# Kernel optimization log

Measured on AMD Instinct MI355X. Metric: run time of the kernel, lower is better.

## Reference

```python
import jax, jax.numpy as jnp
import numpy as np

D_MODEL = 1024
NUM_HEADS = 16
D_K = D_MODEL // NUM_HEADS


def setup_inputs() -> dict:
    key = jax.random.key(0)
    ks = jax.random.split(key, 5)
    s = 1.0 / np.sqrt(D_MODEL)
    return {
        "x": jax.random.normal(ks[0], (2, 2048, D_MODEL), dtype=jnp.float32),
        "Wq": jax.random.normal(ks[1], (D_MODEL, D_MODEL), dtype=jnp.float32) * s,
        "bq": jnp.zeros((D_MODEL,), dtype=jnp.float32),
        "Wk": jax.random.normal(ks[2], (D_MODEL, D_MODEL), dtype=jnp.float32) * s,
        "bk": jnp.zeros((D_MODEL,), dtype=jnp.float32),
        "Wv": jax.random.normal(ks[3], (D_MODEL, D_MODEL), dtype=jnp.float32) * s,
        "bv": jnp.zeros((D_MODEL,), dtype=jnp.float32),
        "Wo": jax.random.normal(ks[4], (D_MODEL, D_MODEL), dtype=jnp.float32) * s,
        "bo": jnp.zeros((D_MODEL,), dtype=jnp.float32),
    }


def reference(x, Wq, bq, Wk, bk, Wv, bv, Wo, bo):
    B, S, D = x.shape
    H, dk = NUM_HEADS, D_K
    Q = x @ Wq + bq  # [B, S, D]
    K = x @ Wk + bk
    V = x @ Wv + bv
    # Faithful to the torch code: plain .view(B, H, S, dk) (NO transpose),
    # i.e. heads are carved out of the flattened (S*D) dim, not the feature dim.
    Q = Q.reshape(B, H, S, dk)
    K = K.reshape(B, H, S, dk)
    V = V.reshape(B, H, S, dk)
    scores = jnp.einsum("bhqd,bhkd->bhqk", Q, K) / jnp.sqrt(jnp.float32(dk))
    attn = jax.nn.softmax(scores, axis=-1)  # [B, H, S, S]
    ctx = jnp.einsum("bhqk,bhkd->bhqd", attn, V)  # [B, H, S, dk]
    out = ctx.reshape(B, S, D) @ Wo + bo
    return out  # dropout is identity in eval mode
```

## Files before the change

### kernel.cpp

```cpp
#include <hip/hip_runtime.h>
#include <hip/hip_bf16.h>
#include <math.h>

#define D_MODEL 1024
#define SEQ     2048
#define BATCH   2
#define NHEAD   16
#define DKH     64
#define BH      (BATCH * NHEAD)

typedef unsigned short u16;
typedef unsigned int   u32;
typedef __bf16 bf16x8 __attribute__((ext_vector_type(8)));
typedef float  f32x4  __attribute__((ext_vector_type(4)));

#define MFMA16(a, b, c) __builtin_amdgcn_mfma_f32_16x16x32_bf16((a), (b), (c), 0, 0, 0)
#define AS1 __attribute__((address_space(1)))
#define AS3 __attribute__((address_space(3)))

#define QSCALE 0.18033688f

__device__ __forceinline__ u16 f2bf(float x) {
    u32 u = __float_as_uint(x);
    u += 0x7fffu + ((u >> 16) & 1u);
    return (u16)(u >> 16);
}
__device__ __forceinline__ float bf2f(u16 b) {
    return __uint_as_float(((u32)b) << 16);
}
__device__ __forceinline__ void gl16(const u16* g, void* lds) {
    __builtin_amdgcn_global_load_lds((const AS1 u32*)g, (AS3 u32*)lds, 16, 0, 0);
}

__global__ __launch_bounds__(256) void conv_all(
    const float* __restrict__ x, u16* __restrict__ Xh, int n4,
    const float* __restrict__ W0, const float* __restrict__ W1,
    const float* __restrict__ W2, const float* __restrict__ W3,
    u16* __restrict__ H0, u16* __restrict__ L0, u16* __restrict__ H1, u16* __restrict__ L1,
    u16* __restrict__ H2, u16* __restrict__ L2, u16* __restrict__ H3, u16* __restrict__ L3)
{
    const int t = threadIdx.x;
    if ((int)blockIdx.x < 4096) {
        int i = blockIdx.x * 256 + t;
        if (i >= n4) return;
        float4 v = reinterpret_cast<const float4*>(x)[i];
        uint2 H;
        H.x = f2bf(v.x) | ((u32)f2bf(v.y) << 16);
        H.y = f2bf(v.z) | ((u32)f2bf(v.w) << 16);
        reinterpret_cast<uint2*>(Xh)[i] = H;
        return;
    }
    int id = blockIdx.x - 4096;
    int bx = id & 15, by = (id >> 4) & 15, bz = id >> 8;
    const float* W; u16 *Ht, *Lt;
    if (bz == 0)      { W = W0; Ht = H0; Lt = L0; }
    else if (bz == 1) { W = W1; Ht = H1; Lt = L1; }
    else if (bz == 2) { W = W2; Ht = H2; Lt = L2; }
    else              { W = W3; Ht = H3; Lt = L3; }

    __shared__ float T[64][65];
    const int n0 = bx * 64, k0 = by * 64;
    #pragma unroll
    for (int i = 0; i < 4; ++i) {
        int f = t + i * 256;
        int kr = f >> 4, ns = (f & 15) * 4;
        float4 v = *reinterpret_cast<const float4*>(&W[(size_t)(k0 + kr) * D_MODEL + n0 + ns]);
        T[kr][ns + 0] = v.x; T[kr][ns + 1] = v.y; T[kr][ns + 2] = v.z; T[kr][ns + 3] = v.w;
    }
    __syncthreads();
    #pragma unroll
    for (int i = 0; i < 4; ++i) {
        int f = t + i * 256;
        int nr = f >> 4, ks = (f & 15) * 4;
        u16 hh[4], ll[4];
        #pragma unroll
        for (int j = 0; j < 4; ++j) {
            float xv = T[ks + j][nr];
            u16 hb = f2bf(xv);
            hh[j] = hb;
            ll[j] = f2bf(xv - bf2f(hb));
        }
        uint2 H, L;
        H.x = hh[0] | ((u32)hh[1] << 16); H.y = hh[2] | ((u32)hh[3] << 16);
        L.x = ll[0] | ((u32)ll[1] << 16); L.y = ll[2] | ((u32)ll[3] << 16);
        size_t o = (size_t)(n0 + nr) * D_MODEL + k0 + ks;
        *reinterpret_cast<uint2*>(&Ht[o]) = H;
        *reinterpret_cast<uint2*>(&Lt[o]) = L;
    }
}

__global__ __launch_bounds__(512, 2) void gemm_qkv(
    const u16* __restrict__ AhG,
    const u16* __restrict__ Bqh, const u16* __restrict__ Bql,
    const u16* __restrict__ Bkh, const u16* __restrict__ Bkl,
    const u16* __restrict__ Bvh, const u16* __restrict__ Bvl,
    const float* __restrict__ bq, const float* __restrict__ bk, const float* __restrict__ bv,
    u16* __restrict__ Qb, u16* __restrict__ Kb, u16* __restrict__ Vb)
{
    constexpr int K = D_MODEL, N = D_MODEL;
    __shared__ u16 LB[2][28672];

    const int tid  = threadIdx.x;
    const int wv   = tid >> 6;
    const int lane = tid & 63;
    const int quad = lane >> 4;
    const int l16  = lane & 15;
    const int wm   = wv & 1, wn = wv >> 1;
    const int brow = blockIdx.y * 128, bcol = blockIdx.x * 128;

    const u16* sp[7];
    int sldb[7];
    #pragma unroll
    for (int j = 0; j < 7; ++j) {
        int c = (j < 3) ? (wv * 3 + j)
              : (j < 5) ? (24 + wv * 2 + (j - 3))
                        : (40 + wv * 2 + (j - 5));
        int a = c >> 3, cc = c & 7;
        int row = cc * 16 + (lane >> 2);
        int gseg = (lane & 3) ^ ((lane >> 3) & 3);
        const u16* p;
        if (a == 0)      p = AhG;
        else if (a == 1) p = Bqh;
        else if (a == 2) p = Bql;
        else if (a == 3) p = Bkh;
        else if (a == 4) p = Bkl;
        else if (a == 5) p = Bvh;
        else             p = Bvl;
        int rbase = (a == 0) ? brow : bcol;
        sp[j]   = p + (size_t)(rbase + row) * K + gseg * 8;
        sldb[j] = a * 8192 + cc * 1024;
    }

    int aro[4], bro[2];
    #pragma unroll
    for (int i = 0; i < 4; ++i) {
        int mr = wm * 64 + i * 16 + l16;
        aro[i] = mr * 64 + ((quad ^ ((mr >> 1) & 3)) * 16);
    }
    #pragma unroll
    for (int i = 0; i < 2; ++i) {
        int nr = wn * 32 + i * 16 + l16;
        bro[i] = nr * 64 + ((quad ^ ((nr >> 1) & 3)) * 16);
    }

    f32x4 acc[3][4][2] = {};

    auto rdB = [&](int cur, int m, bf16x8 (&bh)[2], bf16x8 (&bl)[2]) {
        const int bbh = (1 + 2 * m) * 8192, bbl = (2 + 2 * m) * 8192;
        #pragma unroll
        for (int i = 0; i < 2; ++i) {
            bh[i] = *reinterpret_cast<const bf16x8*>((const char*)LB[cur] + bbh + bro[i]);
            bl[i] = *reinterpret_cast<const bf16x8*>((const char*)LB[cur] + bbl + bro[i]);
        }
    };
    auto mm = [&](int m, bf16x8 (&ah)[4], bf16x8 (&bh)[2], bf16x8 (&bl)[2]) {
        __builtin_amdgcn_s_setprio(1);
        #pragma unroll
        for (int mi = 0; mi < 4; ++mi)
            #pragma unroll
            for (int ni = 0; ni < 2; ++ni) {
                f32x4 c = acc[m][mi][ni];
                c = MFMA16(ah[mi], bh[ni], c);
                c = MFMA16(ah[mi], bl[ni], c);
                acc[m][mi][ni] = c;
            }
        __builtin_amdgcn_s_setprio(0);
    };

    #pragma unroll
    for (int j = 0; j < 7; ++j)
        gl16(sp[j], (char*)LB[0] + sldb[j]);

    for (int it = 0; it < K / 32 - 1; ++it) {
        const int cur = it & 1, nx = cur ^ 1;
        const int k1 = (it + 1) * 32;
        bf16x8 ah[4], bh[2], bl[2];

        asm volatile("s_waitcnt vmcnt(4)" ::: "memory");
        __builtin_amdgcn_s_barrier();
        #pragma unroll
        for (int i = 0; i < 4; ++i)
            ah[i] = *reinterpret_cast<const bf16x8*>((const char*)LB[cur] + aro[i]);
        rdB(cur, 0, bh, bl);
        gl16(sp[0] + k1, (char*)LB[nx] + sldb[0]);
        gl16(sp[1] + k1, (char*)LB[nx] + sldb[1]);
        gl16(sp[2] + k1, (char*)LB[nx] + sldb[2]);
        mm(0, ah, bh, bl);

        asm volatile("s_waitcnt vmcnt(5)" ::: "memory");
        __builtin_amdgcn_s_barrier();
        rdB(cur, 1, bh, bl);
        gl16(sp[3] + k1, (char*)LB[nx] + sldb[3]);
        gl16(sp[4] + k1, (char*)LB[nx] + sldb[4]);
        mm(1, ah, bh, bl);

        asm volatile("s_waitcnt vmcnt(5)" ::: "memory");
        __builtin_amdgcn_s_barrier();
        rdB(cur, 2, bh, bl);
        gl16(sp[5] + k1, (char*)LB[nx] + sldb[5]);
        gl16(sp[6] + k1, (char*)LB[nx] + sldb[6]);
        mm(2, ah, bh, bl);
    }

    {
        const int cur = (K / 32 - 1) & 1;
        bf16x8 ah[4], bh[2], bl[2];

        asm volatile("s_waitcnt vmcnt(4)" ::: "memory");
        __builtin_amdgcn_s_barrier();
        #pragma unroll
        for (int i = 0; i < 4; ++i)
            ah[i] = *reinterpret_cast<const bf16x8*>((const char*)LB[cur] + aro[i]);
        rdB(cur, 0, bh, bl);
        mm(0, ah, bh, bl);

        asm volatile("s_waitcnt vmcnt(2)" ::: "memory");
        __builtin_amdgcn_s_barrier();
        rdB(cur, 1, bh, bl);
        mm(1, ah, bh, bl);

        asm volatile("s_waitcnt vmcnt(0)" ::: "memory");
        __builtin_amdgcn_s_barrier();
        rdB(cur, 2, bh, bl);
        mm(2, ah, bh, bl);
    }

    #pragma unroll
    for (int m = 0; m < 3; ++m) {
        const float* bias = (m == 0) ? bq : (m == 1) ? bk : bv;
        u16* out = (m == 0) ? Qb : (m == 1) ? Kb : Vb;
        const float sc = (m == 0) ? QSCALE : 1.0f;
        #pragma unroll
        for (int mi = 0; mi < 4; ++mi) {
            #pragma unroll
            for (int ni = 0; ni < 2; ++ni) {
                int col = bcol + wn * 32 + ni * 16 + l16;
                float bvv = bias[col];
                #pragma unroll
                for (int r = 0; r < 4; ++r) {
                    int row = brow + wm * 64 + mi * 16 + quad * 4 + r;
                    out[(size_t)row * N + col] = f2bf((acc[m][mi][ni][r] + bvv) * sc);
                }
            }
        }
    }
}

__global__ __launch_bounds__(512, 2) void gemm_oproj(
    const u16* __restrict__ AhG, const u16* __restrict__ Bh, const u16* __restrict__ Bl,
    const float* __restrict__ bias, float* __restrict__ Cf)
{
    constexpr int K = D_MODEL, N = D_MODEL;
    __shared__ u16 LB[2][12288];

    const int tid  = threadIdx.x;
    const int wv   = tid >> 6;
    const int lane = tid & 63;
    const int quad = lane >> 4;
    const int l16  = lane & 15;
    const int wm   = wv & 1, wn = wv >> 1;
    const int brow = blockIdx.y * 128, bcol = blockIdx.x * 128;

    const u16* sp[3];
    int sldb[3];
    #pragma unroll
    for (int j = 0; j < 3; ++j) {
        int c = wv * 3 + j, a = c >> 3, cc = c & 7;
        int row = cc * 16 + (lane >> 2);
        int gseg = (lane & 3) ^ ((lane >> 3) & 3);
        const u16* p = (a == 0) ? AhG : (a == 1) ? Bh : Bl;
        int rbase = (a == 0) ? brow : bcol;
        sp[j]   = p + (size_t)(rbase + row) * K + gseg * 8;
        sldb[j] = a * 8192 + cc * 1024;
    }

    int aro[4], bro[2];
    #pragma unroll
    for (int i = 0; i < 4; ++i) {
        int mr = wm * 64 + i * 16 + l16;
        aro[i] = mr * 64 + ((quad ^ ((mr >> 1) & 3)) * 16);
    }
    #pragma unroll
    for (int i = 0; i < 2; ++i) {
        int nr = wn * 32 + i * 16 + l16;
        bro[i] = nr * 64 + ((quad ^ ((nr >> 1) & 3)) * 16);
    }

    f32x4 acc[4][2] = {};

    #pragma unroll
    for (int j = 0; j < 3; ++j)
        gl16(sp[j], (char*)LB[0] + sldb[j]);

    for (int it = 0; it < K / 32; ++it) {
        const int cur = it & 1;
        __syncthreads();
        if (it + 1 < K / 32) {
            const int nxt = cur ^ 1;
            const int k1 = (it + 1) * 32;
            #pragma unroll
            for (int j = 0; j < 3; ++j)
                gl16(sp[j] + k1, (char*)LB[nxt] + sldb[j]);
        }

        bf16x8 ah[4], bh[2], bl[2];
        #pragma unroll
        for (int i = 0; i < 4; ++i)
            ah[i] = *reinterpret_cast<const bf16x8*>((const char*)LB[cur] + aro[i]);
        #pragma unroll
        for (int i = 0; i < 2; ++i) {
            bh[i] = *reinterpret_cast<const bf16x8*>((const char*)LB[cur] + 8192 + bro[i]);
            bl[i] = *reinterpret_cast<const bf16x8*>((const char*)LB[cur] + 16384 + bro[i]);
        }
        #pragma unroll
        for (int mi = 0; mi < 4; ++mi)
            #pragma unroll
            for (int ni = 0; ni < 2; ++ni) {
                f32x4 c = acc[mi][ni];
                c = MFMA16(ah[mi], bh[ni], c);
                c = MFMA16(ah[mi], bl[ni], c);
                acc[mi][ni] = c;
            }
    }

    #pragma unroll
    for (int mi = 0; mi < 4; ++mi) {
        #pragma unroll
        for (int ni = 0; ni < 2; ++ni) {
            int col = bcol + wn * 32 + ni * 16 + l16;
            float bvv = bias[col];
            #pragma unroll
            for (int r = 0; r < 4; ++r) {
                int row = brow + wm * 64 + mi * 16 + quad * 4 + r;
                Cf[(size_t)row * N + col] = acc[mi][ni][r] + bvv;
            }
        }
    }
}

__global__ __launch_bounds__(256) void v_transpose(
    const u16* __restrict__ V, u16* __restrict__ Vt)
{
    __shared__ u16 T[64][72];
    const int bh = blockIdx.y, st = blockIdx.x;
    const u16* src = V + ((size_t)bh * SEQ + (size_t)st * 64) * 64;
    const int t = threadIdx.x;
    #pragma unroll
    for (int i = 0; i < 2; ++i) {
        int c  = t + i * 256;
        int s  = c >> 3;
        int d0 = (c & 7) * 8;
        uint4 v = reinterpret_cast<const uint4*>(src)[c];
        u16 e[8];
        e[0] = (u16)(v.x & 0xffff); e[1] = (u16)(v.x >> 16);
        e[2] = (u16)(v.y & 0xffff); e[3] = (u16)(v.y >> 16);
        e[4] = (u16)(v.z & 0xffff); e[5] = (u16)(v.z >> 16);
        e[6] = (u16)(v.w & 0xffff); e[7] = (u16)(v.w >> 16);
        #pragma unroll
        for (int j = 0; j < 8; ++j) T[d0 + j][s] = e[j];
    }
    __syncthreads();
    const int d = t >> 2, seg = t & 3;
    u16* dst = Vt + (size_t)bh * 64 * SEQ + (size_t)d * SEQ + st * 64 + seg * 16;
    uint4 a = *reinterpret_cast<const uint4*>(&T[d][seg * 16]);
    uint4 b = *reinterpret_cast<const uint4*>(&T[d][seg * 16 + 8]);
    reinterpret_cast<uint4*>(dst)[0] = a;
    reinterpret_cast<uint4*>(dst)[1] = b;
}

__global__ __launch_bounds__(256, 2) void attn_mfma(
    const u16* __restrict__ Qb_g, const u16* __restrict__ Kb_g,
    const u16* __restrict__ Vt_g, u16* __restrict__ Ch_g)
{
    __shared__ u16 KVS[3][8192];
    __shared__ u16 Pb [128 * 72];

    const int tid  = threadIdx.x;
    const int wv   = tid >> 6;
    const int lane = tid & 63;
    const int quad = lane >> 4;
    const int l16  = lane & 15;
    const int id   = blockIdx.x;
    const int bh   = id & 31;
    const int qt   = id >> 5;

    const size_t qbase = ((size_t)bh * SEQ + (size_t)qt * 128) * 64;
    const size_t kbh   = (size_t)bh * SEQ * 64;
    const size_t vtbh  = (size_t)bh * 64 * SEQ;

    bf16x8 qf[2][2];
    #pragma unroll
    for (int sub = 0; sub < 2; ++sub)
        #pragma unroll
        for (int ks = 0; ks < 2; ++ks) {
            size_t o = qbase + (size_t)(wv * 32 + sub * 16 + l16) * 64 + ks * 32 + quad * 8;
            qf[sub][ks] = *reinterpret_cast<const bf16x8*>(Qb_g + o);
        }

    const u16* sp[4];
    size_t sstep[4];
    int sldb[4];
    #pragma unroll
    for (int j = 0; j < 4; ++j) {
        int c   = wv * 4 + j;
        int arr = c >> 3, cc = c & 7;
        int row = cc * 8 + (lane >> 3);
        int sg  = (lane & 7) ^ (row & 7);
        if (arr == 0) { sp[j] = Kb_g + kbh + (size_t)row * 64 + sg * 8;   sstep[j] = 4096; }
        else          { sp[j] = Vt_g + vtbh + (size_t)row * SEQ + sg * 8; sstep[j] = 64; }
        sldb[j] = arr * 8192 + cc * 1024;
    }

    int fro[4][2];
    #pragma unroll
    for (int t = 0; t < 4; ++t)
        #pragma unroll
        for (int ks = 0; ks < 2; ++ks)
            fro[t][ks] = (t * 16 + l16) * 128 + (((ks * 4 + quad) ^ (l16 & 7)) * 16);

    bf16x8 onesv;
    #pragma unroll
    for (int i = 0; i < 8; ++i) onesv[i] = (__bf16)1.0f;

    f32x4 oacc[2][4] = {};
    f32x4 lsum[2] = {};

    auto S_step = [&](int bufidx, f32x4 (&sacc)[2][4]) {
        const char* kb = (const char*)KVS[bufidx];
        #pragma unroll
        for (int t4 = 0; t4 < 4; ++t4) {
            bf16x8 kh0 = *reinterpret_cast<const bf16x8*>(kb + fro[t4][0]);
            bf16x8 kh1 = *reinterpret_cast<const bf16x8*>(kb + fro[t4][1]);
            #pragma unroll
            for (int sub = 0; sub < 2; ++sub) {
                f32x4 a = sacc[sub][t4];
                a = MFMA16(qf[sub][0], kh0, a);
                a = MFMA16(qf[sub][1], kh1, a);
                sacc[sub][t4] = a;
            }
        }
    };

    auto PV_step = [&](int bufidx) {
        const char* vb = (const char*)KVS[bufidx] + 8192;
        bf16x8 bvf[4][2];
        #pragma unroll
        for (int dt = 0; dt < 4; ++dt) {
            bvf[dt][0] = *reinterpret_cast<const bf16x8*>(vb + fro[dt][0]);
            bvf[dt][1] = *reinterpret_cast<const bf16x8*>(vb + fro[dt][1]);
        }
        #pragma unroll
        for (int sub = 0; sub < 2; ++sub) {
            bf16x8 ap[2];
            #pragma unroll
            for (int ks = 0; ks < 2; ++ks)
                ap[ks] = *reinterpret_cast<const bf16x8*>(
                    &Pb[(wv * 32 + sub * 16 + l16) * 72 + ks * 32 + quad * 8]);
            #pragma unroll
            for (int dt = 0; dt < 4; ++dt) {
                oacc[sub][dt] = MFMA16(ap[0], bvf[dt][0], oacc[sub][dt]);
                oacc[sub][dt] = MFMA16(ap[1], bvf[dt][1], oacc[sub][dt]);
            }
            lsum[sub] = MFMA16(ap[0], onesv, lsum[sub]);
            lsum[sub] = MFMA16(ap[1], onesv, lsum[sub]);
        }
    };

    auto EXP2_step = [&](f32x4 (&sacc)[2][4]) {
        #pragma unroll
        for (int sub = 0; sub < 2; ++sub) {
            int rowb = wv * 32 + sub * 16 + quad * 4;
            #pragma unroll
            for (int r = 0; r < 4; ++r) {
                u32 u0 = __float_as_uint(__builtin_amdgcn_exp2f(sacc[sub][0][r]));
                u32 u1 = __float_as_uint(__builtin_amdgcn_exp2f(sacc[sub][1][r]));
                u32 u2 = __float_as_uint(__builtin_amdgcn_exp2f(sacc[sub][2][r]));
                u32 u3 = __float_as_uint(__builtin_amdgcn_exp2f(sacc[sub][3][r]));
                int ro = (rowb + r) * 72 + l16;
                Pb[ro +  0] = (u16)(u0 >> 16);
                Pb[ro + 16] = (u16)(u1 >> 16);
                Pb[ro + 32] = (u16)(u2 >> 16);
                Pb[ro + 48] = (u16)(u3 >> 16);
            }
        }
    };

    #pragma unroll
    for (int j = 0; j < 4; ++j)
        gl16(sp[j], (char*)KVS[0] + sldb[j]);

    {
        __syncthreads();
        #pragma unroll
        for (int j = 0; j < 4; ++j)
            gl16(sp[j] + sstep[j], (char*)KVS[1] + sldb[j]);
        f32x4 sacc[2][4] = {};
        __builtin_amdgcn_s_setprio(1);
        S_step(0, sacc);
        __builtin_amdgcn_s_setprio(0);
        EXP2_step(sacc);
    }

    int cur = 1, prv = 0, nxt = 2;
    for (int kt = 1; kt < SEQ / 64; ++kt) {
        __syncthreads();
        if (kt + 1 < SEQ / 64) {
            #pragma unroll
            for (int j = 0; j < 4; ++j)
                gl16(sp[j] + (size_t)(kt + 1) * sstep[j], (char*)KVS[nxt] + sldb[j]);
        }

        f32x4 sacc[2][4] = {};
        __builtin_amdgcn_s_setprio(1);
        S_step(cur, sacc);
        PV_step(prv);
        __builtin_amdgcn_s_setprio(0);
        EXP2_step(sacc);

        prv = cur; cur = nxt; nxt = (nxt == 2) ? 0 : nxt + 1;
    }

    __builtin_amdgcn_s_setprio(1);
    PV_step(prv);
    __builtin_amdgcn_s_setprio(0);

    u16* Oh = Ch_g + qbase;
    #pragma unroll
    for (int sub = 0; sub < 2; ++sub) {
        float inv[4];
        #pragma unroll
        for (int r = 0; r < 4; ++r) inv[r] = 1.0f / lsum[sub][r];
        #pragma unroll
        for (int dt = 0; dt < 4; ++dt)
            #pragma unroll
            for (int r = 0; r < 4; ++r) {
                int row = wv * 32 + sub * 16 + quad * 4 + r;
                Oh[(size_t)row * 64 + dt * 16 + l16] = f2bf(oacc[sub][dt][r] * inv[r]);
            }
    }
}

extern "C" void kernel_launch(void* const* d_in, const int* in_sizes, int n_in,
                              void* d_out, int out_size, void* d_ws, size_t ws_size,
                              hipStream_t stream)
{
    const float* x  = (const float*)d_in[0];
    const float* Wq = (const float*)d_in[1];
    const float* bq = (const float*)d_in[2];
    const float* Wk = (const float*)d_in[3];
    const float* bk = (const float*)d_in[4];
    const float* Wv = (const float*)d_in[5];
    const float* bv = (const float*)d_in[6];
    const float* Wo = (const float*)d_in[7];
    const float* bo = (const float*)d_in[8];
    float* out = (float*)d_out;

    const int M = BATCH * SEQ;
    const int N = D_MODEL;
    const size_t NE = (size_t)M * N;
    const size_t NW = (size_t)N * N;

    u16* w16 = (u16*)d_ws;
    u16* Xh   = w16;
    u16* Qb   = Xh   + NE;
    u16* Kb   = Qb   + NE;
    u16* Vb   = Kb   + NE;
    u16* Vtb  = Vb   + NE;
    u16* Ctxh = Vtb  + NE;
    u16* WTqh = Ctxh + NE;
    u16* WTql = WTqh + NW;
    u16* WTkh = WTql + NW;
    u16* WTkl = WTkh + NW;
    u16* WTvh = WTkl + NW;
    u16* WTvl = WTvh + NW;
    u16* WToh = WTvl + NW;
    u16* WTol = WToh + NW;

    conv_all<<<dim3(4096 + 1024), dim3(256), 0, stream>>>(
        x, Xh, (int)(NE / 4),
        Wq, Wk, Wv, Wo, WTqh, WTql, WTkh, WTkl, WTvh, WTvl, WToh, WTol);

    gemm_qkv<<<dim3(N / 128, M / 128), dim3(512), 0, stream>>>(
        Xh, WTqh, WTql, WTkh, WTkl, WTvh, WTvl, bq, bk, bv, Qb, Kb, Vb);

    v_transpose<<<dim3(SEQ / 64, BH), dim3(256), 0, stream>>>(Vb, Vtb);

    attn_mfma<<<dim3((SEQ / 128) * BH), dim3(256), 0, stream>>>(Qb, Kb, Vtb, Ctxh);

    gemm_oproj<<<dim3(N / 128, M / 128), dim3(512), 0, stream>>>(
        Ctxh, WToh, WTol, bo, out);
}
```

Measured before the change: 212.8 us.

## Split attention work across eight waves and pack P and V-transpose stores

The attention kernel now runs 512 threads per block, so each wave handles 16 query rows instead of 32. This halves per-wave accumulator registers and raises the number of waves available to hide latency. The cost is that each K/V fragment read from LDS now feeds half as many MFMAs. The softmax P tile is written as packed 64-bit words using a permuted key order, and the V-transpose kernel writes V in the same permuted order so P·V stays consistent. This replaces scattered 16-bit LDS stores with wider ones.

```diff
diff --git a/kernel.cpp b/kernel.cpp
--- a/kernel.cpp
+++ b/kernel.cpp
@@ -361,14 +361,24 @@
     }
     __syncthreads();
     const int d = t >> 2, seg = t & 3;
-    u16* dst = Vt + (size_t)bh * 64 * SEQ + (size_t)d * SEQ + st * 64 + seg * 16;
-    uint4 a = *reinterpret_cast<const uint4*>(&T[d][seg * 16]);
-    uint4 b = *reinterpret_cast<const uint4*>(&T[d][seg * 16 + 8]);
-    reinterpret_cast<uint4*>(dst)[0] = a;
-    reinterpret_cast<uint4*>(dst)[1] = b;
-}
-
-__global__ __launch_bounds__(256, 2) void attn_mfma(
+    u16* dst = Vt + (size_t)bh * 64 * SEQ + (size_t)d * SEQ + st * 64;
+    #pragma unroll
+    for (int gg = 0; gg < 2; ++gg) {
+        int g = seg * 2 + gg;
+        u32 r0 = *reinterpret_cast<const u32*>(&T[d][2 * g]);
+        u32 r1 = *reinterpret_cast<const u32*>(&T[d][2 * g + 16]);
+        u32 r2 = *reinterpret_cast<const u32*>(&T[d][2 * g + 32]);
+        u32 r3 = *reinterpret_cast<const u32*>(&T[d][2 * g + 48]);
+        uint4 w;
+        w.x = (r0 & 0xffffu) | (r1 << 16);
+        w.y = (r2 & 0xffffu) | (r3 << 16);
+        w.z = (r0 >> 16) | (r1 & 0xffff0000u);
+        w.w = (r2 >> 16) | (r3 & 0xffff0000u);
+        *reinterpret_cast<uint4*>(&dst[8 * g]) = w;
+    }
+}
+
+__global__ __launch_bounds__(512, 4) void attn_mfma(
     const u16* __restrict__ Qb_g, const u16* __restrict__ Kb_g,
     const u16* __restrict__ Vt_g, u16* __restrict__ Ch_g)
 {
@@ -383,26 +393,25 @@
     const int id   = blockIdx.x;
     const int bh   = id & 31;
     const int qt   = id >> 5;
+    const int qrow = wv * 16;
 
     const size_t qbase = ((size_t)bh * SEQ + (size_t)qt * 128) * 64;
     const size_t kbh   = (size_t)bh * SEQ * 64;
     const size_t vtbh  = (size_t)bh * 64 * SEQ;
 
-    bf16x8 qf[2][2];
-    #pragma unroll
-    for (int sub = 0; sub < 2; ++sub)
-        #pragma unroll
-        for (int ks = 0; ks < 2; ++ks) {
-            size_t o = qbase + (size_t)(wv * 32 + sub * 16 + l16) * 64 + ks * 32 + quad * 8;
-            qf[sub][ks] = *reinterpret_cast<const bf16x8*>(Qb_g + o);
-        }
-
-    const u16* sp[4];
-    size_t sstep[4];
-    int sldb[4];
-    #pragma unroll
-    for (int j = 0; j < 4; ++j) {
-        int c   = wv * 4 + j;
+    bf16x8 qf[2];
+    #pragma unroll
+    for (int ks = 0; ks < 2; ++ks) {
+        size_t o = qbase + (size_t)(qrow + l16) * 64 + ks * 32 + quad * 8;
+        qf[ks] = *reinterpret_cast<const bf16x8*>(Qb_g + o);
+    }
+
+    const u16* sp[2];
+    size_t sstep[2];
+    int sldb[2];
+    #pragma unroll
+    for (int j = 0; j < 2; ++j) {
+        int c   = wv * 2 + j;
         int arr = c >> 3, cc = c & 7;
         int row = cc * 8 + (lane >> 3);
         int sg  = (lane & 7) ^ (row & 7);
@@ -422,22 +431,19 @@
     #pragma unroll
     for (int i = 0; i < 8; ++i) onesv[i] = (__bf16)1.0f;
 
-    f32x4 oacc[2][4] = {};
-    f32x4 lsum[2] = {};
-
-    auto S_step = [&](int bufidx, f32x4 (&sacc)[2][4]) {
+    f32x4 oacc[4] = {};
+    f32x4 lsum = {};
+
+    auto S_step = [&](int bufidx, f32x4 (&sacc)[4]) {
         const char* kb = (const char*)KVS[bufidx];
         #pragma unroll
         for (int t4 = 0; t4 < 4; ++t4) {
             bf16x8 kh0 = *reinterpret_cast<const bf16x8*>(kb + fro[t4][0]);
             bf16x8 kh1 = *reinterpret_cast<const bf16x8*>(kb + fro[t4][1]);
-            #pragma unroll
-            for (int sub = 0; sub < 2; ++sub) {
-                f32x4 a = sacc[sub][t4];
-                a = MFMA16(qf[sub][0], kh0, a);
-                a = MFMA16(qf[sub][1], kh1, a);
-                sacc[sub][t4] = a;
-            }
+            f32x4 a = sacc[t4];
+            a = MFMA16(qf[0], kh0, a);
+            a = MFMA16(qf[1], kh1, a);
+            sacc[t4] = a;
         }
     };
 
@@ -449,52 +455,45 @@
             bvf[dt][0] = *reinterpret_cast<const bf16x8*>(vb + fro[dt][0]);
             bvf[dt][1] = *reinterpret_cast<const bf16x8*>(vb + fro[dt][1]);
         }
-        #pragma unroll
-        for (int sub = 0; sub < 2; ++sub) {
-            bf16x8 ap[2];
-            #pragma unroll
-            for (int ks = 0; ks < 2; ++ks)
-                ap[ks] = *reinterpret_cast<const bf16x8*>(
-                    &Pb[(wv * 32 + sub * 16 + l16) * 72 + ks * 32 + quad * 8]);
-            #pragma unroll
-            for (int dt = 0; dt < 4; ++dt) {
-                oacc[sub][dt] = MFMA16(ap[0], bvf[dt][0], oacc[sub][dt]);
-                oacc[sub][dt] = MFMA16(ap[1], bvf[dt][1], oacc[sub][dt]);
-            }
-            lsum[sub] = MFMA16(ap[0], onesv, lsum[sub]);
-            lsum[sub] = MFMA16(ap[1], onesv, lsum[sub]);
-        }
+        bf16x8 ap[2];
+        #pragma unroll
+        for (int ks = 0; ks < 2; ++ks)
+            ap[ks] = *reinterpret_cast<const bf16x8*>(
+                &Pb[(qrow + l16) * 72 + ks * 32 + quad * 8]);
+        #pragma unroll
+        for (int dt = 0; dt < 4; ++dt) {
+            oacc[dt] = MFMA16(ap[0], bvf[dt][0], oacc[dt]);
+            oacc[dt] = MFMA16(ap[1], bvf[dt][1], oacc[dt]);
+        }
+        lsum = MFMA16(ap[0], onesv, lsum);
+        lsum = MFMA16(ap[1], onesv, lsum);
     };
 
-    auto EXP2_step = [&](f32x4 (&sacc)[2][4]) {
-        #pragma unroll
-        for (int sub = 0; sub < 2; ++sub) {
-            int rowb = wv * 32 + sub * 16 + quad * 4;
-            #pragma unroll
-            for (int r = 0; r < 4; ++r) {
-                u32 u0 = __float_as_uint(__builtin_amdgcn_exp2f(sacc[sub][0][r]));
-                u32 u1 = __float_as_uint(__builtin_amdgcn_exp2f(sacc[sub][1][r]));
-                u32 u2 = __float_as_uint(__builtin_amdgcn_exp2f(sacc[sub][2][r]));
-                u32 u3 = __float_as_uint(__builtin_amdgcn_exp2f(sacc[sub][3][r]));
-                int ro = (rowb + r) * 72 + l16;
-                Pb[ro +  0] = (u16)(u0 >> 16);
-                Pb[ro + 16] = (u16)(u1 >> 16);
-                Pb[ro + 32] = (u16)(u2 >> 16);
-                Pb[ro + 48] = (u16)(u3 >> 16);
-            }
+    auto EXP2_step = [&](f32x4 (&sacc)[4]) {
+        const int rowb = qrow + quad * 4;
+        #pragma unroll
+        for (int r = 0; r < 4; ++r) {
+            u32 u0 = __float_as_uint(__builtin_amdgcn_exp2f(sacc[0][r]));
+            u32 u1 = __float_as_uint(__builtin_amdgcn_exp2f(sacc[1][r]));
+            u32 u2 = __float_as_uint(__builtin_amdgcn_exp2f(sacc[2][r]));
+            u32 u3 = __float_as_uint(__builtin_amdgcn_exp2f(sacc[3][r]));
+            uint2 w;
+            w.x = (u0 >> 16) | (u1 & 0xffff0000u);
+            w.y = (u2 >> 16) | (u3 & 0xffff0000u);
+            *reinterpret_cast<uint2*>(&Pb[(rowb + r) * 72 + l16 * 4]) = w;
         }
     };
 
     #pragma unroll
-    for (int j = 0; j < 4; ++j)
+    for (int j = 0; j < 2; ++j)
         gl16(sp[j], (char*)KVS[0] + sldb[j]);
 
     {
         __syncthreads();
         #pragma unroll
-        for (int j = 0; j < 4; ++j)
+        for (int j = 0; j < 2; ++j)
             gl16(sp[j] + sstep[j], (char*)KVS[1] + sldb[j]);
-        f32x4 sacc[2][4] = {};
+        f32x4 sacc[4] = {};
         __builtin_amdgcn_s_setprio(1);
         S_step(0, sacc);
         __builtin_amdgcn_s_setprio(0);
@@ -506,11 +505,11 @@
         __syncthreads();
         if (kt + 1 < SEQ / 64) {
             #pragma unroll
-            for (int j = 0; j < 4; ++j)
+            for (int j = 0; j < 2; ++j)
                 gl16(sp[j] + (size_t)(kt + 1) * sstep[j], (char*)KVS[nxt] + sldb[j]);
         }
 
-        f32x4 sacc[2][4] = {};
+        f32x4 sacc[4] = {};
         __builtin_amdgcn_s_setprio(1);
         S_step(cur, sacc);
         PV_step(prv);
@@ -525,19 +524,16 @@
     __builtin_amdgcn_s_setprio(0);
 
     u16* Oh = Ch_g + qbase;
-    #pragma unroll
-    for (int sub = 0; sub < 2; ++sub) {
-        float inv[4];
-        #pragma unroll
-        for (int r = 0; r < 4; ++r) inv[r] = 1.0f / lsum[sub][r];
-        #pragma unroll
-        for (int dt = 0; dt < 4; ++dt)
-            #pragma unroll
-            for (int r = 0; r < 4; ++r) {
-                int row = wv * 32 + sub * 16 + quad * 4 + r;
-                Oh[(size_t)row * 64 + dt * 16 + l16] = f2bf(oacc[sub][dt][r] * inv[r]);
-            }
-    }
+    float inv[4];
+    #pragma unroll
+    for (int r = 0; r < 4; ++r) inv[r] = 1.0f / lsum[r];
+    #pragma unroll
+    for (int dt = 0; dt < 4; ++dt)
+        #pragma unroll
+        for (int r = 0; r < 4; ++r) {
+            int row = qrow + quad * 4 + r;
+            Oh[(size_t)row * 64 + dt * 16 + l16] = f2bf(oacc[dt][r] * inv[r]);
+        }
 }
 
 extern "C" void kernel_launch(void* const* d_in, const int* in_sizes, int n_in,
@@ -585,7 +581,7 @@
 
     v_transpose<<<dim3(SEQ / 64, BH), dim3(256), 0, stream>>>(Vb, Vtb);
 
-    attn_mfma<<<dim3((SEQ / 128) * BH), dim3(256), 0, stream>>>(Qb, Kb, Vtb, Ctxh);
+    attn_mfma<<<dim3((SEQ / 128) * BH), dim3(512), 0, stream>>>(Qb, Kb, Vtb, Ctxh);
 
     gemm_oproj<<<dim3(N / 128, M / 128), dim3(512), 0, stream>>>(
         Ctxh, WToh, WTol, bo, out);
```

Result: no change. 211.9 us (-0.4%).
